# Kernel tuning notes

Measured on AMD Instinct MI355X. Metric: run time of the kernel, lower is better.

## Reference

```python
import jax, jax.numpy as jnp
import numpy as np
import math

NUM_HEADS = 16
D_MODEL = 1024
D_HEAD = D_MODEL // NUM_HEADS
B, S = 2, 2048


def setup_inputs() -> dict:
    key = jax.random.key(0)
    k1, k2 = jax.random.split(key)
    query = jax.random.normal(k1, (B, S, D_MODEL), dtype=jnp.float32)
    # causal mask: True where masked (j > i)
    mask = jnp.broadcast_to(jnp.triu(jnp.ones((S, S), dtype=bool), k=1), (B, S, S))
    W_o = jax.random.normal(k2, (D_MODEL, D_MODEL), dtype=jnp.float32) * (1.0 / math.sqrt(D_MODEL))
    b_o = jnp.zeros((D_MODEL,), dtype=jnp.float32)
    return {"query": query, "mask": mask, "W_o": W_o, "b_o": b_o}


def reference(query, mask, W_o, b_o):
    # NOTE: faithful to source — q/k/v linear layers are never applied in forward.
    # Self-attention: key = value = query.
    Bq, Sq, D = query.shape
    # split heads: [B, S, D] -> [B, H, S, dh]
    q = query.reshape(Bq, Sq, NUM_HEADS, D_HEAD).transpose(0, 2, 1, 3)
    k = q
    v = q
    # logits: [B, H, Sq, Sk]
    logits = jnp.einsum("bhqd,bhkd->bhqk", q, k) / math.sqrt(D_HEAD)
    logits = jnp.where(mask[:, None, :, :], -jnp.inf, logits)
    attn = jax.nn.softmax(logits, axis=-1)          # [B, H, Sq, Sk]
    out = jnp.einsum("bhqk,bhkd->bhqd", attn, v)    # [B, H, Sq, dh]
    # merge heads: [B, Sq, D]
    out = out.transpose(0, 2, 1, 3).reshape(Bq, Sq, D)
    # output projection (torch Linear: x @ W.T + b)
    return out @ W_o.T + b_o
```

## Files before the change

kernel.cpp:

```cpp
#include <hip/hip_runtime.h>
#include <hip/hip_bf16.h>
#include <stdint.h>

#define SEQ 2048
#define DMODEL 1024

typedef __attribute__((ext_vector_type(8))) short short8;
typedef __attribute__((ext_vector_type(4))) short short4v;
typedef __attribute__((ext_vector_type(4))) float floatx4;

__device__ __forceinline__ floatx4 mfma16x16x32(short8 a, short8 b, floatx4 c) {
  return __builtin_amdgcn_mfma_f32_16x16x32_bf16(a, b, c, 0, 0, 0);
}

__device__ __forceinline__ floatx4 mfma16x16x16(short4v a, short4v b, floatx4 c) {
  return __builtin_amdgcn_mfma_f32_16x16x16bf16_1k(a, b, c, 0, 0, 0);
}

__device__ __forceinline__ uint16_t f2bf(float x) {
  __hip_bfloat16 h = __float2bfloat16(x);
  return *reinterpret_cast<uint16_t*>(&h);
}

__device__ __forceinline__ uint16_t f2bf_fast(float x) {
  union { float f; uint32_t u; } c; c.f = x;
  return (uint16_t)((c.u + 0x8000u) >> 16);
}

__device__ __forceinline__ float bf2f(uint16_t u) {
  uint32_t x = (uint32_t)u << 16;
  union { uint32_t u; float f; } c; c.u = x; return c.f;
}

__device__ __forceinline__ void glds16(const uint16_t* g, uint16_t* l) {
  __builtin_amdgcn_global_load_lds(
      (const __attribute__((address_space(1))) uint32_t*)g,
      (__attribute__((address_space(3))) uint32_t*)(uint32_t)(uintptr_t)l,
      16, 0, 0);
}

__global__ __launch_bounds__(256) void cvt_kernel(
    const float* __restrict__ q, uint16_t* __restrict__ qd,
    const float* __restrict__ w, uint16_t* __restrict__ wd,
    int nq4, int ntot4) {
  int i = blockIdx.x * 256 + threadIdx.x;
  if (i >= ntot4) return;
  const float* src = (i < nq4) ? q : w;
  uint16_t* dst = (i < nq4) ? qd : wd;
  int j = (i < nq4) ? i : i - nq4;
  float4 v = ((const float4*)src)[j];
  ushort4 r;
  r.x = f2bf(v.x); r.y = f2bf(v.y); r.z = f2bf(v.z); r.w = f2bf(v.w);
  ((ushort4*)dst)[j] = r;
}

__device__ __forceinline__ int vt_idx(int d, int key) {
  return d * 64 + ((((key >> 3) ^ (d >> 3) ^ d) & 7) << 3) + (key & 7);
}

__global__ __launch_bounds__(256, 2) void attn_kernel(
    const uint16_t* __restrict__ qbf, uint16_t* __restrict__ Opart,
    float* __restrict__ Lpart) {
  const int p    = blockIdx.x >> 5;
  const int bh   = blockIdx.x & 31;
  const int b    = bh >> 4;
  const int h    = bh & 15;
  const int tid  = threadIdx.x;
  const int wave = tid >> 6;
  const int lane = tid & 63;
  const int l15  = lane & 15;
  const int quad = lane >> 4;

  __shared__ uint16_t Kt[2][64 * 64];
  __shared__ uint16_t Vt[2][64 * 64];

  const uint16_t* base = qbf + (size_t)b * SEQ * DMODEL + h * 64;

  const int r0 = tid >> 3;
  const int cg = (tid & 7) * 8;
  const int krow = tid >> 3;
  const int kcg  = tid & 7;

  auto stage = [&](int kt, int buf) {
    #pragma unroll
    for (int rr = 0; rr < 2; ++rr) {
      int row = rr * 32 + krow;
      glds16(base + (size_t)(kt * 64 + row) * DMODEL + ((kcg ^ (row & 7)) * 8),
             &Kt[buf][row * 64 + kcg * 8]);
    }
    uint4 v0 = *(const uint4*)(base + (size_t)(kt * 64 + 2 * r0) * DMODEL + cg);
    uint4 v1 = *(const uint4*)(base + (size_t)(kt * 64 + 2 * r0 + 1) * DMODEL + cg);
    uint16_t t0[8], t1[8];
    *(uint4*)t0 = v0;
    *(uint4*)t1 = v1;
    #pragma unroll
    for (int i = 0; i < 8; ++i) {
      uint32_t pk = (uint32_t)t0[i] | ((uint32_t)t1[i] << 16);
      *(uint32_t*)&Vt[buf][vt_idx(cg + i, 2 * r0)] = pk;
    }
  };

  auto run_unit = [&](int qt, int half, bool first) {
    const int ktlo = half ? (qt + 1) : 0;
    const int kthi = half ? (2 * qt + 1) : qt;

    short8 qf[2][2];
    #pragma unroll
    for (int s = 0; s < 2; ++s)
      #pragma unroll
      for (int ks = 0; ks < 2; ++ks)
        qf[s][ks] = *(const short8*)(base +
            (size_t)(qt * 128 + s * 64 + wave * 16 + l15) * DMODEL + ks * 32 + quad * 8);

    floatx4 o_acc[2][4];
    float l_run[2];
    #pragma unroll
    for (int s = 0; s < 2; ++s) {
      #pragma unroll
      for (int dt = 0; dt < 4; ++dt) o_acc[s][dt] = (floatx4){0.f, 0.f, 0.f, 0.f};
      l_run[s] = 0.f;
    }

    if (!first) __syncthreads();
    stage(ktlo, ktlo & 1);

    auto iter = [&](int kt, int nt0, int nt1, bool d0, bool d1) {
      __syncthreads();
      if (kt < kthi) stage(kt + 1, (kt + 1) & 1);
      const int buf = kt & 1;

      floatx4 sacc[2][4];
      #pragma unroll
      for (int s = 0; s < 2; ++s)
        #pragma unroll
        for (int nt = 0; nt < 4; ++nt) sacc[s][nt] = (floatx4){0.f, 0.f, 0.f, 0.f};

      #pragma unroll
      for (int ks = 0; ks < 2; ++ks)
        #pragma unroll
        for (int nt = 0; nt < 4; ++nt) {
          if (nt > nt0 && nt > nt1) continue;
          int row = nt * 16 + l15;
          short8 kf = *(const short8*)
              &Kt[buf][row * 64 + (((ks * 4 + quad) ^ (row & 7)) * 8)];
          if (nt <= nt0) sacc[0][nt] = mfma16x16x32(kf, qf[0][ks], sacc[0][nt]);
          if (nt <= nt1) sacc[1][nt] = mfma16x16x32(kf, qf[1][ks], sacc[1][nt]);
        }

      #pragma unroll
      for (int nt = 0; nt < 4; ++nt) {
        if (nt > nt0 && nt > nt1) continue;
        short4v vf[4];
        #pragma unroll
        for (int dt = 0; dt < 4; ++dt)
          vf[dt] = *(const short4v*)&Vt[buf][vt_idx(dt * 16 + l15, nt * 16 + quad * 4)];
        #pragma unroll
        for (int s = 0; s < 2; ++s) {
          const int ntm = s ? nt1 : nt0;
          const bool dg = s ? d1 : d0;
          if (nt > ntm) continue;
          short4v pf;
          #pragma unroll
          for (int r = 0; r < 4; ++r) {
            float pp = __builtin_amdgcn_exp2f(fmaf(sacc[s][nt][r], 0.1803369f, -10.f));
            if (dg && nt == wave && quad * 4 + r > l15) pp = 0.f;
            l_run[s] += pp;
            pf[r] = (short)f2bf_fast(pp);
          }
          #pragma unroll
          for (int dt = 0; dt < 4; ++dt)
            o_acc[s][dt] = mfma16x16x16(pf, vf[dt], o_acc[s][dt]);
        }
      }
    };

    if (half == 0) {
      if (qt == 0) {
        iter(0, wave, 3, true, false);
      } else {
        for (int kt = 0; kt <= qt; ++kt) iter(kt, 3, 3, false, false);
      }
    } else {
      for (int kt = qt + 1; kt < 2 * qt; ++kt) iter(kt, 3, 3, false, false);
      if (qt >= 1) iter(2 * qt, wave, 3, true, false);
      iter(2 * qt + 1, -1, wave, false, true);
    }

    const size_t obase = (size_t)half * (4096 * 1024);
    #pragma unroll
    for (int s = 0; s < 2; ++s) {
      float l = l_run[s];
      l += __shfl_xor(l, 16, 64);
      l += __shfl_xor(l, 32, 64);
      int rowg = b * SEQ + qt * 128 + s * 64 + wave * 16 + l15;
      if (quad == 0) Lpart[half * 65536 + h * 4096 + rowg] = l;
      #pragma unroll
      for (int dt = 0; dt < 4; ++dt)
        #pragma unroll
        for (int r = 0; r < 4; ++r) {
          int rowo = b * SEQ + qt * 128 + s * 64 + wave * 16 + quad * 4 + r;
          Opart[obase + (size_t)rowo * DMODEL + h * 64 + dt * 16 + l15] =
              f2bf_fast(o_acc[s][dt][r]);
        }
    }
  };

  run_unit(p, 0, true);
  run_unit(15 - p, 1, false);
}

__global__ __launch_bounds__(256) void combine_kernel(
    const uint16_t* __restrict__ Opart, const float* __restrict__ Lpart,
    uint16_t* __restrict__ X) {
  int i = blockIdx.x * 256 + threadIdx.x;
  int row = i >> 7;
  int c8  = (i & 127) * 8;
  int h   = c8 >> 6;
  float inv = 1.0f / (Lpart[h * 4096 + row] + Lpart[65536 + h * 4096 + row]);
  uint16_t a[8], bpt[8], o[8];
  *(uint4*)a   = *(const uint4*)&Opart[(size_t)row * DMODEL + c8];
  *(uint4*)bpt = *(const uint4*)&Opart[(size_t)4096 * 1024 + (size_t)row * DMODEL + c8];
  #pragma unroll
  for (int k = 0; k < 8; ++k)
    o[k] = f2bf_fast((bf2f(a[k]) + bf2f(bpt[k])) * inv);
  *(uint4*)&X[(size_t)row * DMODEL + c8] = *(uint4*)o;
}

__global__ __launch_bounds__(256, 4) void proj_kernel(
    const uint16_t* __restrict__ X, const uint16_t* __restrict__ Wo,
    const float* __restrict__ bo, float* __restrict__ out) {
  const int bx = blockIdx.x;
  const int by = blockIdx.y;
  const int tid = threadIdx.x;
  const int wave = tid >> 6, lane = tid & 63, l15 = lane & 15, quad = lane >> 4;
  const int wr = wave >> 1, wc = wave & 1;

  __shared__ uint16_t As[2][128 * 64];
  __shared__ uint16_t Bs[2][64 * 64];

  floatx4 acc[4][2];
  #pragma unroll
  for (int mt = 0; mt < 4; ++mt)
    #pragma unroll
    for (int nt = 0; nt < 2; ++nt) acc[mt][nt] = (floatx4){0.f, 0.f, 0.f, 0.f};

  const int srow = tid >> 3;
  const int scg  = tid & 7;

  auto stage = [&](int kt, int buf) {
    #pragma unroll
    for (int rr = 0; rr < 4; ++rr) {
      int row = rr * 32 + srow;
      glds16(X + (size_t)(bx * 128 + row) * DMODEL + kt * 64 + ((scg ^ (row & 7)) * 8),
             &As[buf][row * 64 + scg * 8]);
    }
    #pragma unroll
    for (int rr = 0; rr < 2; ++rr) {
      int row = rr * 32 + srow;
      glds16(Wo + (size_t)(by * 64 + row) * DMODEL + kt * 64 + ((scg ^ (row & 7)) * 8),
             &Bs[buf][row * 64 + scg * 8]);
    }
  };

  stage(0, 0);
  for (int kt = 0; kt < 16; ++kt) {
    __syncthreads();
    if (kt < 15) stage(kt + 1, (kt + 1) & 1);
    const int buf = kt & 1;
    #pragma unroll
    for (int ks = 0; ks < 2; ++ks) {
      short8 af[4], bf2[2];
      #pragma unroll
      for (int mt = 0; mt < 4; ++mt) {
        int row = wr * 64 + mt * 16 + l15;
        af[mt] = *(const short8*)
            &As[buf][row * 64 + (((ks * 4 + quad) ^ (row & 7)) * 8)];
      }
      #pragma unroll
      for (int nt = 0; nt < 2; ++nt) {
        int row = wc * 32 + nt * 16 + l15;
        bf2[nt] = *(const short8*)
            &Bs[buf][row * 64 + (((ks * 4 + quad) ^ (row & 7)) * 8)];
      }
      #pragma unroll
      for (int mt = 0; mt < 4; ++mt)
        #pragma unroll
        for (int nt = 0; nt < 2; ++nt)
          acc[mt][nt] = mfma16x16x32(af[mt], bf2[nt], acc[mt][nt]);
    }
  }

  #pragma unroll
  for (int nt = 0; nt < 2; ++nt) {
    int colg = by * 64 + wc * 32 + nt * 16 + l15;
    float bias = bo[colg];
    #pragma unroll
    for (int mt = 0; mt < 4; ++mt)
      #pragma unroll
      for (int r2 = 0; r2 < 4; ++r2) {
        int rowg = bx * 128 + wr * 64 + mt * 16 + quad * 4 + r2;
        out[(size_t)rowg * DMODEL + colg] = acc[mt][nt][r2] + bias;
      }
  }
}

extern "C" void kernel_launch(void* const* d_in, const int* in_sizes, int n_in,
                              void* d_out, int out_size, void* d_ws, size_t ws_size,
                              hipStream_t stream) {
  const float* q_f32  = (const float*)d_in[0];
  const float* Wo_f32 = (const float*)d_in[2];
  const float* bo     = (const float*)d_in[3];
  float* out = (float*)d_out;

  uint16_t* qbf   = (uint16_t*)d_ws;
  uint16_t* X     = (uint16_t*)((char*)d_ws + (size_t)8 * 1024 * 1024);
  uint16_t* wobf  = (uint16_t*)((char*)d_ws + (size_t)16 * 1024 * 1024);
  uint16_t* Opart = (uint16_t*)((char*)d_ws + (size_t)18 * 1024 * 1024);
  float*    Lpart = (float*)((char*)d_ws + (size_t)34 * 1024 * 1024);

  const int nq4 = 2 * SEQ * DMODEL / 4;
  const int nw4 = DMODEL * DMODEL / 4;
  const int nt4 = nq4 + nw4;
  cvt_kernel<<<dim3((nt4 + 255) / 256), dim3(256), 0, stream>>>(
      q_f32, qbf, Wo_f32, wobf, nq4, nt4);

  attn_kernel<<<dim3(512), dim3(256), 0, stream>>>(qbf, Opart, Lpart);
  combine_kernel<<<dim3(2048), dim3(256), 0, stream>>>(Opart, Lpart, X);
  proj_kernel<<<dim3(32, 16), dim3(256), 0, stream>>>(X, wobf, bo, out);
}
```

Before: 141.9 us.

## Stage key/value tiles in pairs to halve barrier count per loop

Double-buffers pairs of 64-key K/V tiles instead of single tiles, so each __syncthreads and prefetch step covers two tiles of compute. Mask parameters are now derived inside the tile routine from kt rather than passed by the caller. This is meant to cut barrier and issue overhead and deepen the prefetch. In exchange, LDS use doubles to 64KB per block, which may limit occupancy against launch_bounds(256,2), and register pressure from holding two V loads rises.

Measured after the change: 147.1 us. 3.7% more time.

```diff
diff --git a/kernel.cpp b/kernel.cpp
--- a/kernel.cpp
+++ b/kernel.cpp
@@ -71,8 +71,8 @@
   const int l15  = lane & 15;
   const int quad = lane >> 4;
 
-  __shared__ uint16_t Kt[2][64 * 64];
-  __shared__ uint16_t Vt[2][64 * 64];
+  __shared__ uint16_t Kt[2][2][64 * 64];
+  __shared__ uint16_t Vt[2][2][64 * 64];
 
   const uint16_t* base = qbf + (size_t)b * SEQ * DMODEL + h * 64;
 
@@ -81,23 +81,37 @@
   const int krow = tid >> 3;
   const int kcg  = tid & 7;
 
-  auto stage = [&](int kt, int buf) {
+  auto kstage = [&](int kt, int pb, int slot) {
     #pragma unroll
     for (int rr = 0; rr < 2; ++rr) {
       int row = rr * 32 + krow;
       glds16(base + (size_t)(kt * 64 + row) * DMODEL + ((kcg ^ (row & 7)) * 8),
-             &Kt[buf][row * 64 + kcg * 8]);
-    }
-    uint4 v0 = *(const uint4*)(base + (size_t)(kt * 64 + 2 * r0) * DMODEL + cg);
-    uint4 v1 = *(const uint4*)(base + (size_t)(kt * 64 + 2 * r0 + 1) * DMODEL + cg);
+             &Kt[pb][slot][row * 64 + kcg * 8]);
+    }
+  };
+  auto vwrite = [&](uint4 v0, uint4 v1, int pb, int slot) {
     uint16_t t0[8], t1[8];
     *(uint4*)t0 = v0;
     *(uint4*)t1 = v1;
     #pragma unroll
     for (int i = 0; i < 8; ++i) {
       uint32_t pk = (uint32_t)t0[i] | ((uint32_t)t1[i] << 16);
-      *(uint32_t*)&Vt[buf][vt_idx(cg + i, 2 * r0)] = pk;
-    }
+      *(uint32_t*)&Vt[pb][slot][vt_idx(cg + i, 2 * r0)] = pk;
+    }
+  };
+  auto stage_pair = [&](int k0, int klim, int pb) {
+    kstage(k0, pb, 0);
+    bool two = (k0 + 1 <= klim);
+    if (two) kstage(k0 + 1, pb, 1);
+    uint4 a0 = *(const uint4*)(base + (size_t)(k0 * 64 + 2 * r0) * DMODEL + cg);
+    uint4 a1 = *(const uint4*)(base + (size_t)(k0 * 64 + 2 * r0 + 1) * DMODEL + cg);
+    uint4 b0, b1;
+    if (two) {
+      b0 = *(const uint4*)(base + (size_t)((k0 + 1) * 64 + 2 * r0) * DMODEL + cg);
+      b1 = *(const uint4*)(base + (size_t)((k0 + 1) * 64 + 2 * r0 + 1) * DMODEL + cg);
+    }
+    vwrite(a0, a1, pb, 0);
+    if (two) vwrite(b0, b1, pb, 1);
   };
 
   auto run_unit = [&](int qt, int half, bool first) {
@@ -122,12 +136,13 @@
     }
 
     if (!first) __syncthreads();
-    stage(ktlo, ktlo & 1);
-
-    auto iter = [&](int kt, int nt0, int nt1, bool d0, bool d1) {
-      __syncthreads();
-      if (kt < kthi) stage(kt + 1, (kt + 1) & 1);
-      const int buf = kt & 1;
+    stage_pair(ktlo, kthi, 0);
+
+    auto tile_compute = [&](int kt, int pb, int slot) {
+      int nt0, nt1; bool d0, d1;
+      if (kt < 2 * qt)       { nt0 = 3;    nt1 = 3;    d0 = false; d1 = false; }
+      else if (kt == 2 * qt) { nt0 = wave; nt1 = 3;    d0 = true;  d1 = false; }
+      else                   { nt0 = -1;   nt1 = wave; d0 = false; d1 = true;  }
 
       floatx4 sacc[2][4];
       #pragma unroll
@@ -142,7 +157,7 @@
           if (nt > nt0 && nt > nt1) continue;
           int row = nt * 16 + l15;
           short8 kf = *(const short8*)
-              &Kt[buf][row * 64 + (((ks * 4 + quad) ^ (row & 7)) * 8)];
+              &Kt[pb][slot][row * 64 + (((ks * 4 + quad) ^ (row & 7)) * 8)];
           if (nt <= nt0) sacc[0][nt] = mfma16x16x32(kf, qf[0][ks], sacc[0][nt]);
           if (nt <= nt1) sacc[1][nt] = mfma16x16x32(kf, qf[1][ks], sacc[1][nt]);
         }
@@ -153,7 +168,8 @@
         short4v vf[4];
         #pragma unroll
         for (int dt = 0; dt < 4; ++dt)
-          vf[dt] = *(const short4v*)&Vt[buf][vt_idx(dt * 16 + l15, nt * 16 + quad * 4)];
+          vf[dt] = *(const short4v*)
+              &Vt[pb][slot][vt_idx(dt * 16 + l15, nt * 16 + quad * 4)];
         #pragma unroll
         for (int s = 0; s < 2; ++s) {
           const int ntm = s ? nt1 : nt0;
@@ -174,16 +190,13 @@
       }
     };
 
-    if (half == 0) {
-      if (qt == 0) {
-        iter(0, wave, 3, true, false);
-      } else {
-        for (int kt = 0; kt <= qt; ++kt) iter(kt, 3, 3, false, false);
-      }
-    } else {
-      for (int kt = qt + 1; kt < 2 * qt; ++kt) iter(kt, 3, 3, false, false);
-      if (qt >= 1) iter(2 * qt, wave, 3, true, false);
-      iter(2 * qt + 1, -1, wave, false, true);
+    int pb = 0;
+    for (int kt0 = ktlo; kt0 <= kthi; kt0 += 2) {
+      __syncthreads();
+      if (kt0 + 2 <= kthi) stage_pair(kt0 + 2, kthi, pb ^ 1);
+      tile_compute(kt0, pb, 0);
+      if (kt0 + 1 <= kthi) tile_compute(kt0 + 1, pb, 1);
+      pb ^= 1;
     }
 
     const size_t obase = (size_t)half * (4096 * 1024);
```

## Split each attention work pair across two blocks to double grid size

Applied to the files above, without the earlier changes.

Attention work is now split into 1024 blocks instead of 512. Each original paired unit (query tile p and its mirror 15-p) is divided at key-tile 8, so two blocks share the key range and write into four partial output and L slots. The combine kernel sums two to four partials per row, depending on the query tile. This is meant to raise occupancy and balance across the MI355X's CUs, at the cost of extra partial-output traffic, a larger workspace, and more combine work.

Result: slower. 153.5 us (+8.2%).

```diff
diff --git a/kernel.cpp b/kernel.cpp
--- a/kernel.cpp
+++ b/kernel.cpp
@@ -61,7 +61,9 @@
 __global__ __launch_bounds__(256, 2) void attn_kernel(
     const uint16_t* __restrict__ qbf, uint16_t* __restrict__ Opart,
     float* __restrict__ Lpart) {
-  const int p    = blockIdx.x >> 5;
+  const int pj   = blockIdx.x >> 5;
+  const int p    = pj >> 1;
+  const int j    = pj & 1;
   const int bh   = blockIdx.x & 31;
   const int b    = bh >> 4;
   const int h    = bh & 15;
@@ -100,9 +102,10 @@
     }
   };
 
-  auto run_unit = [&](int qt, int half, bool first) {
-    const int ktlo = half ? (qt + 1) : 0;
-    const int kthi = half ? (2 * qt + 1) : qt;
+  bool ran = false;
+
+  auto run_segment = [&](int qt, int ktlo, int kthi, int slot) {
+    if (ktlo > kthi) return;
 
     short8 qf[2][2];
     #pragma unroll
@@ -121,13 +124,19 @@
       l_run[s] = 0.f;
     }
 
-    if (!first) __syncthreads();
+    if (ran) __syncthreads();
+    ran = true;
     stage(ktlo, ktlo & 1);
 
-    auto iter = [&](int kt, int nt0, int nt1, bool d0, bool d1) {
+    for (int kt = ktlo; kt <= kthi; ++kt) {
       __syncthreads();
       if (kt < kthi) stage(kt + 1, (kt + 1) & 1);
       const int buf = kt & 1;
+
+      int nt0, nt1; bool d0, d1;
+      if (kt < 2 * qt)       { nt0 = 3;    nt1 = 3;    d0 = false; d1 = false; }
+      else if (kt == 2 * qt) { nt0 = wave; nt1 = 3;    d0 = true;  d1 = false; }
+      else                   { nt0 = -1;   nt1 = wave; d0 = false; d1 = true;  }
 
       floatx4 sacc[2][4];
       #pragma unroll
@@ -172,28 +181,16 @@
             o_acc[s][dt] = mfma16x16x16(pf, vf[dt], o_acc[s][dt]);
         }
       }
-    };
-
-    if (half == 0) {
-      if (qt == 0) {
-        iter(0, wave, 3, true, false);
-      } else {
-        for (int kt = 0; kt <= qt; ++kt) iter(kt, 3, 3, false, false);
-      }
-    } else {
-      for (int kt = qt + 1; kt < 2 * qt; ++kt) iter(kt, 3, 3, false, false);
-      if (qt >= 1) iter(2 * qt, wave, 3, true, false);
-      iter(2 * qt + 1, -1, wave, false, true);
-    }
-
-    const size_t obase = (size_t)half * (4096 * 1024);
+    }
+
+    const size_t obase = (size_t)slot * (4096 * 1024);
     #pragma unroll
     for (int s = 0; s < 2; ++s) {
       float l = l_run[s];
       l += __shfl_xor(l, 16, 64);
       l += __shfl_xor(l, 32, 64);
       int rowg = b * SEQ + qt * 128 + s * 64 + wave * 16 + l15;
-      if (quad == 0) Lpart[half * 65536 + h * 4096 + rowg] = l;
+      if (quad == 0) Lpart[slot * 65536 + h * 4096 + rowg] = l;
       #pragma unroll
       for (int dt = 0; dt < 4; ++dt)
         #pragma unroll
@@ -205,8 +202,17 @@
     }
   };
 
-  run_unit(p, 0, true);
-  run_unit(15 - p, 1, false);
+  {
+    int a_lo = j ? 8 : 0;
+    int a_hi = j ? p : (p < 7 ? p : 7);
+    run_segment(p, a_lo, a_hi, j);
+  }
+  {
+    int qb = 15 - p;
+    int ilo = j ? (p + 1 > 8 ? p + 1 : 8) : p + 1;
+    int ihi = j ? 16 : 7;
+    run_segment(qb, 15 - 2 * p + ilo, 15 - 2 * p + ihi, 2 + j);
+  }
 }
 
 __global__ __launch_bounds__(256) void combine_kernel(
@@ -216,13 +222,35 @@
   int row = i >> 7;
   int c8  = (i & 127) * 8;
   int h   = c8 >> 6;
-  float inv = 1.0f / (Lpart[h * 4096 + row] + Lpart[65536 + h * 4096 + row]);
-  uint16_t a[8], bpt[8], o[8];
-  *(uint4*)a   = *(const uint4*)&Opart[(size_t)row * DMODEL + c8];
-  *(uint4*)bpt = *(const uint4*)&Opart[(size_t)4096 * 1024 + (size_t)row * DMODEL + c8];
-  #pragma unroll
-  for (int k = 0; k < 8; ++k)
-    o[k] = f2bf_fast((bf2f(a[k]) + bf2f(bpt[k])) * inv);
+  int qt  = (row & 2047) >> 7;
+  float lsum = Lpart[h * 4096 + row] + Lpart[3 * 65536 + h * 4096 + row];
+  float acc[8];
+  uint16_t a[8];
+  *(uint4*)a = *(const uint4*)&Opart[(size_t)row * DMODEL + c8];
+  #pragma unroll
+  for (int k = 0; k < 8; ++k) acc[k] = bf2f(a[k]);
+  *(uint4*)a = *(const uint4*)
+      &Opart[(size_t)3 * 4096 * 1024 + (size_t)row * DMODEL + c8];
+  #pragma unroll
+  for (int k = 0; k < 8; ++k) acc[k] += bf2f(a[k]);
+  if (qt >= 8) {
+    lsum += Lpart[65536 + h * 4096 + row];
+    *(uint4*)a = *(const uint4*)
+        &Opart[(size_t)4096 * 1024 + (size_t)row * DMODEL + c8];
+    #pragma unroll
+    for (int k = 0; k < 8; ++k) acc[k] += bf2f(a[k]);
+  }
+  if (qt >= 9) {
+    lsum += Lpart[2 * 65536 + h * 4096 + row];
+    *(uint4*)a = *(const uint4*)
+        &Opart[(size_t)2 * 4096 * 1024 + (size_t)row * DMODEL + c8];
+    #pragma unroll
+    for (int k = 0; k < 8; ++k) acc[k] += bf2f(a[k]);
+  }
+  float inv = 1.0f / lsum;
+  uint16_t o[8];
+  #pragma unroll
+  for (int k = 0; k < 8; ++k) o[k] = f2bf_fast(acc[k] * inv);
   *(uint4*)&X[(size_t)row * DMODEL + c8] = *(uint4*)o;
 }
 
@@ -316,7 +344,7 @@
   uint16_t* X     = (uint16_t*)((char*)d_ws + (size_t)8 * 1024 * 1024);
   uint16_t* wobf  = (uint16_t*)((char*)d_ws + (size_t)16 * 1024 * 1024);
   uint16_t* Opart = (uint16_t*)((char*)d_ws + (size_t)18 * 1024 * 1024);
-  float*    Lpart = (float*)((char*)d_ws + (size_t)34 * 1024 * 1024);
+  float*    Lpart = (float*)((char*)d_ws + (size_t)50 * 1024 * 1024);
 
   const int nq4 = 2 * SEQ * DMODEL / 4;
   const int nw4 = DMODEL * DMODEL / 4;
@@ -324,7 +352,7 @@
   cvt_kernel<<<dim3((nt4 + 255) / 256), dim3(256), 0, stream>>>(
       q_f32, qbf, Wo_f32, wobf, nq4, nt4);
 
-  attn_kernel<<<dim3(512), dim3(256), 0, stream>>>(qbf, Opart, Lpart);
+  attn_kernel<<<dim3(1024), dim3(256), 0, stream>>>(qbf, Opart, Lpart);
   combine_kernel<<<dim3(2048), dim3(256), 0, stream>>>(Opart, Lpart, X);
   proj_kernel<<<dim3(32, 16), dim3(256), 0, stream>>>(X, wobf, bo, out);
 }
```
